# Optimization experiments

Hardware: AMD Instinct MI355X
Metric: run time of the kernel (lower is better)

The kernel has to match this reference:

```python
import jax, jax.numpy as jnp
import numpy as np

P = 2          # SamplesLoss p=2
BLUR = 0.05    # eps_final = BLUR**P = 0.0025
SCALING = 0.8  # annealing factor per iteration (on the blur scale)


def _cost(x, y):
    # geomloss cost for p=2: |x - y|^2 / 2, shape (N, M)
    x2 = jnp.sum(x * x, axis=-1)
    y2 = jnp.sum(y * y, axis=-1)
    return 0.5 * (x2[:, None] + y2[None, :] - 2.0 * (x @ y.T))


def _softmin(eps, C, h):
    # -eps * log sum_j exp(h_j - C_ij / eps); h already contains log-weights
    return -eps * jax.nn.logsumexp(h[None, :] - C / eps, axis=1)


def _eps_schedule(x, y):
    # geomloss scaling_parameters / epsilon_schedule with diameter from bounding box
    xn, yn = np.asarray(x), np.asarray(y)
    mins = np.minimum(xn.min(0), yn.min(0))
    maxs = np.maximum(xn.max(0), yn.max(0))
    diameter = float(np.linalg.norm(maxs - mins))
    eps_list = ([diameter ** P]
                + [float(np.exp(e)) for e in np.arange(P * np.log(diameter), P * np.log(BLUR), P * np.log(SCALING))]
                + [BLUR ** P])
    return eps_list


def _sinkhorn_divergence(x, y, eps_list):
    # Debiased Sinkhorn divergence S_eps(x, y), geomloss sinkhorn_tensorized
    N, M = x.shape[0], y.shape[0]
    sg = jax.lax.stop_gradient
    C_xy, C_yx = _cost(x, y), _cost(y, x)
    C_xx, C_yy = _cost(x, sg(x)), _cost(y, sg(y))  # geomloss detaches 2nd arg
    # The annealing loop runs with autograd disabled in geomloss:
    Cxy_, Cyx_, Cxx_, Cyy_ = sg(C_xy), sg(C_yx), sg(C_xx), sg(C_yy)
    a_log = jnp.full((N,), -np.log(N), dtype=x.dtype)  # log uniform weights
    b_log = jnp.full((M,), -np.log(M), dtype=y.dtype)
    e0 = eps_list[0]
    f_aa = _softmin(e0, Cxx_, a_log)
    g_bb = _softmin(e0, Cyy_, b_log)
    g_ab = _softmin(e0, Cyx_, a_log)
    f_ba = _softmin(e0, Cxy_, b_log)
    for eps in eps_list:  # fixed schedule, not a data-dim loop
        ft_ba = _softmin(eps, Cxy_, b_log + g_ab / eps)
        gt_ab = _softmin(eps, Cyx_, a_log + f_ba / eps)
        ft_aa = _softmin(eps, Cxx_, a_log + f_aa / eps)
        gt_bb = _softmin(eps, Cyy_, b_log + g_bb / eps)
        f_ba, g_ab = 0.5 * (f_ba + ft_ba), 0.5 * (g_ab + gt_ab)
        f_aa, g_bb = 0.5 * (f_aa + ft_aa), 0.5 * (g_bb + gt_bb)
    # Final extrapolation step (the only one geomloss differentiates through):
    eps = eps_list[-1]
    f_ba, g_ab = (_softmin(eps, C_xy, sg(b_log + g_ab / eps)),
                  _softmin(eps, C_yx, sg(a_log + f_ba / eps)))
    f_aa = _softmin(eps, C_xx, sg(a_log + f_aa / eps))
    g_bb = _softmin(eps, C_yy, sg(b_log + g_bb / eps))
    # scal with uniform weights == mean
    return jnp.mean(f_ba - f_aa) + jnp.mean(g_ab - g_bb)


def setup_inputs() -> dict:
    key = jax.random.key(0)
    kx, kt = jax.random.split(key)
    x = jax.random.normal(kx, (4096, 64), dtype=jnp.float32)
    target = jax.random.normal(kt, (4096, 64), dtype=jnp.float32)
    return {"x": x, "target": target}


def reference(x, target):
    eps_list = _eps_schedule(x, target)  # concrete schedule from data diameter
    return _sinkhorn_divergence(x, target, eps_list)
```

## Files before the change

### kernel.cpp

```cpp
#include <hip/hip_runtime.h>
#include <math.h>

#define NPTS 4096
#define DIM  64
#define MAX_ITERS 40
#define NCHUNK 32
#define TILE 128

#define ALOG (-8.317766166719343f)
#define L2E  (1.4426950408889634f)
#define LN2  (0.6931471805599453f)

#if __has_builtin(__builtin_amdgcn_exp2f)
#define EXP2F(x) __builtin_amdgcn_exp2f(x)
#else
#define EXP2F(x) exp2f(x)
#endif
#if __has_builtin(__builtin_amdgcn_logf)
#define LOG2F(x) __builtin_amdgcn_logf(x)
#else
#define LOG2F(x) log2f(x)
#endif

typedef _Float16 half8 __attribute__((ext_vector_type(8)));

__global__ void minmax_part_kernel(const float* __restrict__ x,
                                   const float* __restrict__ y,
                                   float* __restrict__ partmn,
                                   float* __restrict__ partmx) {
    int t = threadIdx.x;
    int bid = blockIdx.x;
    int g0 = bid * 256 + t;
    const int total = NPTS * DIM;
    float mn = INFINITY, mx = -INFINITY;
    for (int g = g0; g < total; g += 128 * 256) {
        float v = x[g]; mn = fminf(mn, v); mx = fmaxf(mx, v);
        float w = y[g]; mn = fminf(mn, w); mx = fmaxf(mx, w);
    }
    __shared__ float smn[256], smx[256];
    smn[t] = mn; smx[t] = mx;
    __syncthreads();
    if (t < 64) {
        for (int q = 1; q < 4; q++) {
            mn = fminf(mn, smn[t + 64 * q]);
            mx = fmaxf(mx, smx[t + 64 * q]);
        }
        partmn[bid * 64 + t] = mn;
        partmx[bid * 64 + t] = mx;
    }
}

__global__ void schedule_kernel(const float* __restrict__ partmn,
                                const float* __restrict__ partmx,
                                int* __restrict__ hdr,
                                float* __restrict__ sched) {
    int d = threadIdx.x;
    float mn = INFINITY, mx = -INFINITY;
    for (int b = 0; b < 128; b++) {
        mn = fminf(mn, partmn[b * 64 + d]);
        mx = fmaxf(mx, partmx[b * 64 + d]);
    }
    float range = mx - mn;
    __shared__ float r2[64];
    r2[d] = range * range;
    __syncthreads();
    if (d == 0) {
        float ss = 0.f;
        for (int k = 0; k < 64; k++) ss += r2[k];
        float diam_f = sqrtf(ss);
        double diam = (double)diam_f;
        double start = 2.0 * log(diam);
        double stop  = 2.0 * log(0.05);
        double step  = 2.0 * log(0.8);
        int n_ar = (int)ceil((stop - start) / step);
        if (n_ar < 0) n_ar = 0;
        int n_eps = n_ar + 2;
        if (n_eps > 64) n_eps = 64;
        sched[0] = (float)(diam * diam);
        for (int k = 0; k < n_ar && (1 + k) < 63; k++)
            sched[1 + k] = (float)exp(start + step * (double)k);
        sched[n_eps - 1] = 0.0025f;
        for (int k = n_eps; k < 64; k++) sched[k] = 0.0025f;
        hdr[0] = n_eps;
    }
}

__global__ void sqnorm_kernel(const float* __restrict__ X, float* __restrict__ out) {
    int wave = (blockIdx.x * blockDim.x + threadIdx.x) >> 6;
    int lane = threadIdx.x & 63;
    if (wave >= NPTS) return;
    float v = X[wave * DIM + lane];
    float s = v * v;
    for (int o = 32; o > 0; o >>= 1) s += __shfl_xor(s, o, 64);
    if (lane == 0) out[wave] = s;
}

__global__ __launch_bounds__(256) void gram_kernel(const float* __restrict__ A,
                                                   const float* __restrict__ B,
                                                   _Float16* __restrict__ G) {
    __shared__ float As[64][68], Bs[64][68];
    int t = threadIdx.x;
    int i0 = blockIdx.y * 64, j0 = blockIdx.x * 64;
    for (int q = 0; q < 4; q++) {
        int fi = q * 256 + t;
        int r = fi >> 4, c4 = (fi & 15) * 4;
        *(float4*)&As[r][c4] = *(const float4*)&A[(i0 + r) * DIM + c4];
        *(float4*)&Bs[r][c4] = *(const float4*)&B[(j0 + r) * DIM + c4];
    }
    __syncthreads();
    int tx = t & 15, ty = t >> 4;
    float acc[4][4] = {};
    for (int k = 0; k < 64; k++) {
        float a[4], b[4];
#pragma unroll
        for (int u = 0; u < 4; u++) a[u] = As[ty + 16 * u][k];
#pragma unroll
        for (int v = 0; v < 4; v++) b[v] = Bs[tx + 16 * v][k];
#pragma unroll
        for (int u = 0; u < 4; u++)
#pragma unroll
            for (int v = 0; v < 4; v++) acc[u][v] = fmaf(a[u], b[v], acc[u][v]);
    }
    for (int u = 0; u < 4; u++)
        for (int v = 0; v < 4; v++)
            G[(size_t)(i0 + ty + 16 * u) * NPTS + j0 + tx + 16 * v] = (_Float16)acc[u][v];
}

struct TileArgs {
    const _Float16 *Gxy, *Gxx, *Gyy;
    const float *x2, *y2;
    const float *fba, *gab, *faa, *gbb;
    float *PxyR_m, *PxyR_s, *PxyC_m, *PxyC_s;
    float *Pxx_m, *Pxx_s, *Pyy_m, *Pyy_s;
    const int* hdr; const float* sched;
    int t; int mode;
};

__global__ __launch_bounds__(256) void tile_kernel(TileArgs A) {
    int n_eps = A.hdr[0];
    if (A.mode == 1 && A.t >= n_eps) return;
    int idx = (A.t < 0) ? (n_eps - 1) : A.t;
    float eps = A.sched[idx];
    float inv2 = (1.0f / eps) * L2E;

    int b = blockIdx.x;
    const _Float16 *G;
    const float *hc_f, *hc_sq, *hr_f, *hr_sq;
    float *Prm, *Prs, *Pcm, *Pcs;
    int ti, tj; bool diag = false;
    if (b < 1024) {
        ti = b >> 5; tj = b & 31;
        G = A.Gxy;
        hc_f = A.gab; hc_sq = A.y2;
        hr_f = A.fba; hr_sq = A.x2;
        Prm = A.PxyR_m; Prs = A.PxyR_s; Pcm = A.PxyC_m; Pcs = A.PxyC_s;
    } else {
        int u;
        if (b < 1024 + 528) {
            u = b - 1024; G = A.Gxx; hc_f = A.faa; hc_sq = A.x2;
            Prm = A.Pxx_m; Prs = A.Pxx_s; Pcm = A.Pxx_m; Pcs = A.Pxx_s;
        } else {
            u = b - 1552; G = A.Gyy; hc_f = A.gbb; hc_sq = A.y2;
            Prm = A.Pyy_m; Prs = A.Pyy_s; Pcm = A.Pyy_m; Pcs = A.Pyy_s;
        }
        hr_f = hc_f; hr_sq = hc_sq;
        ti = 0; while (u >= NCHUNK - ti) { u -= NCHUNK - ti; ti++; }
        tj = ti + u;
        diag = (ti == tj);
    }
    const float base2 = ALOG * L2E;

    __shared__ float tile[64][65];
    __shared__ float h2c[128], h2r[128];
    __shared__ float red_m[4][64], red_s[4][64];

    int tt = threadIdx.x;
    int gi0 = ti * TILE, gj0 = tj * TILE;
    if (tt < 128) {
        int j = gj0 + tt;
        float f = hc_f ? hc_f[j] : 0.f;
        h2c[tt] = base2 + (f - 0.5f * hc_sq[j]) * inv2;
    } else {
        int i = gi0 + (tt - 128);
        float f = hr_f ? hr_f[i] : 0.f;
        h2r[tt - 128] = base2 + (f - 0.5f * hr_sq[i]) * inv2;
    }

    float rm[2] = {-INFINITY, -INFINITY}, rs[2] = {0.f, 0.f};
    float cm[2] = {-INFINITY, -INFINITY}, cs[2] = {0.f, 0.f};
    int lr = tt & 63, lq = tt >> 6;

    for (int qc = 0; qc < 2; qc++) {
        for (int qr = 0; qr < 2; qr++) {
            __syncthreads();
            {
                const _Float16* src = G + (size_t)(gi0 + qr * 64) * NPTS + gj0 + qc * 64;
                for (int q = 0; q < 2; q++) {
                    int fi = q * 256 + tt;
                    int r = fi >> 3, c8 = (fi & 7) * 8;
                    half8 h = *(const half8*)(src + (size_t)r * NPTS + c8);
#pragma unroll
                    for (int j = 0; j < 8; j++) tile[r][c8 + j] = (float)h[j];
                }
            }
            __syncthreads();
            {
                float v[16], lm = -INFINITY;
#pragma unroll
                for (int k = 0; k < 16; k++) {
                    v[k] = fmaf(tile[lr][lq * 16 + k], inv2, h2c[qc * 64 + lq * 16 + k]);
                    lm = fmaxf(lm, v[k]);
                }
                float nm = fmaxf(rm[qr], lm);
                float acc = rs[qr] * EXP2F(rm[qr] - nm);
#pragma unroll
                for (int k = 0; k < 16; k++) acc += EXP2F(v[k] - nm);
                rm[qr] = nm; rs[qr] = acc;
            }
            if (!diag) {
                float v[16], lm = -INFINITY;
#pragma unroll
                for (int k = 0; k < 16; k++) {
                    v[k] = fmaf(tile[lq * 16 + k][lr], inv2, h2r[qr * 64 + lq * 16 + k]);
                    lm = fmaxf(lm, v[k]);
                }
                float nm = fmaxf(cm[qc], lm);
                float acc = cs[qc] * EXP2F(cm[qc] - nm);
#pragma unroll
                for (int k = 0; k < 16; k++) acc += EXP2F(v[k] - nm);
                cm[qc] = nm; cs[qc] = acc;
            }
        }
    }

    for (int qr = 0; qr < 2; qr++) {
        __syncthreads();
        red_m[lq][lr] = rm[qr]; red_s[lq][lr] = rs[qr];
        __syncthreads();
        if (tt < 64) {
            float M = fmaxf(fmaxf(red_m[0][tt], red_m[1][tt]),
                            fmaxf(red_m[2][tt], red_m[3][tt]));
            float S = red_s[0][tt] * EXP2F(red_m[0][tt] - M)
                    + red_s[1][tt] * EXP2F(red_m[1][tt] - M)
                    + red_s[2][tt] * EXP2F(red_m[2][tt] - M)
                    + red_s[3][tt] * EXP2F(red_m[3][tt] - M);
            int gi = gi0 + qr * 64 + tt;
            Prm[tj * NPTS + gi] = M; Prs[tj * NPTS + gi] = S;
        }
    }
    if (!diag) {
        for (int qc = 0; qc < 2; qc++) {
            __syncthreads();
            red_m[lq][lr] = cm[qc]; red_s[lq][lr] = cs[qc];
            __syncthreads();
            if (tt < 64) {
                float M = fmaxf(fmaxf(red_m[0][tt], red_m[1][tt]),
                                fmaxf(red_m[2][tt], red_m[3][tt]));
                float S = red_s[0][tt] * EXP2F(red_m[0][tt] - M)
                        + red_s[1][tt] * EXP2F(red_m[1][tt] - M)
                        + red_s[2][tt] * EXP2F(red_m[2][tt] - M)
                        + red_s[3][tt] * EXP2F(red_m[3][tt] - M);
                int gj = gj0 + qc * 64 + tt;
                Pcm[ti * NPTS + gj] = M; Pcs[ti * NPTS + gj] = S;
            }
        }
    }
}

struct CombArgs {
    const float *PxyR_m, *PxyR_s, *PxyC_m, *PxyC_s;
    const float *Pxx_m, *Pxx_s, *Pyy_m, *Pyy_s;
    const float *x2, *y2;
    const float *fba_old, *gab_old, *faa_old, *gbb_old;
    float *fba, *gab, *faa, *gbb;
    const int* hdr; const float* sched; int t; int mode;
};

__global__ void comb_kernel(CombArgs A) {
    int vec = blockIdx.x >> 4;
    int r = (blockIdx.x & 15) * 256 + threadIdx.x;
    int n_eps = A.hdr[0];
    const float *Pm, *Ps, *sq, *old; float *out;
    switch (vec) {
        case 0:  Pm = A.PxyR_m; Ps = A.PxyR_s; sq = A.x2; old = A.fba_old; out = A.fba; break;
        case 1:  Pm = A.PxyC_m; Ps = A.PxyC_s; sq = A.y2; old = A.gab_old; out = A.gab; break;
        case 2:  Pm = A.Pxx_m;  Ps = A.Pxx_s;  sq = A.x2; old = A.faa_old; out = A.faa; break;
        default: Pm = A.Pyy_m;  Ps = A.Pyy_s;  sq = A.y2; old = A.gbb_old; out = A.gbb; break;
    }
    if (A.mode == 1 && A.t >= n_eps) { out[r] = old[r]; return; }
    int idx = (A.t < 0) ? (n_eps - 1) : A.t;
    float eps = A.sched[idx];
    float M = -INFINITY;
    for (int q = 0; q < NCHUNK; q++) M = fmaxf(M, Pm[q * NPTS + r]);
    float S = 0.f;
    for (int q = 0; q < NCHUNK; q++) S += Ps[q * NPTS + r] * EXP2F(Pm[q * NPTS + r] - M);
    float res = 0.5f * sq[r] - eps * LN2 * (M + LOG2F(S));
    out[r] = (A.mode == 1) ? 0.5f * (old[r] + res) : res;
}

__global__ void reduce_kernel(const float* __restrict__ fba, const float* __restrict__ faa,
                              const float* __restrict__ gab, const float* __restrict__ gbb,
                              float* __restrict__ out) {
    int t = threadIdx.x;
    double s1 = 0.0, s2 = 0.0;
    for (int i = t; i < NPTS; i += 256) {
        s1 += (double)fba[i] - (double)faa[i];
        s2 += (double)gab[i] - (double)gbb[i];
    }
    __shared__ double sh1[256], sh2[256];
    sh1[t] = s1; sh2[t] = s2;
    __syncthreads();
    for (int o = 128; o > 0; o >>= 1) {
        if (t < o) { sh1[t] += sh1[t + o]; sh2[t] += sh2[t + o]; }
        __syncthreads();
    }
    if (t == 0) out[0] = (float)(sh1[0] / NPTS + sh2[0] / NPTS);
}

extern "C" void kernel_launch(void* const* d_in, const int* in_sizes, int n_in,
                              void* d_out, int out_size, void* d_ws, size_t ws_size,
                              hipStream_t stream) {
    const float* x = (const float*)d_in[0];
    const float* y = (const float*)d_in[1];
    float* out = (float*)d_out;
    float* w = (float*)d_ws;

    int*   hdr   = (int*)w;
    float* sched = w + 16;
    float* pmn   = w + 80;
    float* pmx   = w + 8272;
    float* x2    = w + 16464;
    float* y2    = w + 20560;
    float* st    = w + 24656;
    float* fba[2] = { st,            st + 4096 };
    float* gab[2] = { st + 2*4096,   st + 3*4096 };
    float* faa[2] = { st + 4*4096,   st + 5*4096 };
    float* gbb[2] = { st + 6*4096,   st + 7*4096 };
    float* P = w + 57424;
    float* PxyR_m = P;             float* PxyR_s = P + 131072;
    float* PxyC_m = P + 2*131072;  float* PxyC_s = P + 3*131072;
    float* Pxx_m  = P + 4*131072;  float* Pxx_s  = P + 5*131072;
    float* Pyy_m  = P + 6*131072;  float* Pyy_s  = P + 7*131072;
    const size_t NN = (size_t)NPTS * NPTS;
    _Float16* Gxy = (_Float16*)(w + 2097152);
    _Float16* Gxx = Gxy + NN;
    _Float16* Gyy = Gxx + NN;

    hipLaunchKernelGGL(minmax_part_kernel, dim3(128), dim3(256), 0, stream, x, y, pmn, pmx);
    hipLaunchKernelGGL(schedule_kernel, dim3(1), dim3(64), 0, stream, pmn, pmx, hdr, sched);
    hipLaunchKernelGGL(sqnorm_kernel, dim3(1024), dim3(256), 0, stream, x, x2);
    hipLaunchKernelGGL(sqnorm_kernel, dim3(1024), dim3(256), 0, stream, y, y2);
    hipLaunchKernelGGL(gram_kernel, dim3(64, 64), dim3(256), 0, stream, x, y, Gxy);
    hipLaunchKernelGGL(gram_kernel, dim3(64, 64), dim3(256), 0, stream, x, x, Gxx);
    hipLaunchKernelGGL(gram_kernel, dim3(64, 64), dim3(256), 0, stream, y, y, Gyy);

    const int NBLK = 1024 + 528 + 528;
    TileArgs TA;
    TA.Gxy = Gxy; TA.Gxx = Gxx; TA.Gyy = Gyy;
    TA.x2 = x2; TA.y2 = y2;
    TA.PxyR_m = PxyR_m; TA.PxyR_s = PxyR_s; TA.PxyC_m = PxyC_m; TA.PxyC_s = PxyC_s;
    TA.Pxx_m = Pxx_m; TA.Pxx_s = Pxx_s; TA.Pyy_m = Pyy_m; TA.Pyy_s = Pyy_s;
    TA.hdr = hdr; TA.sched = sched;

    CombArgs CA;
    CA.PxyR_m = PxyR_m; CA.PxyR_s = PxyR_s; CA.PxyC_m = PxyC_m; CA.PxyC_s = PxyC_s;
    CA.Pxx_m = Pxx_m; CA.Pxx_s = Pxx_s; CA.Pyy_m = Pyy_m; CA.Pyy_s = Pyy_s;
    CA.x2 = x2; CA.y2 = y2; CA.hdr = hdr; CA.sched = sched;

    TA.fba = nullptr; TA.gab = nullptr; TA.faa = nullptr; TA.gbb = nullptr;
    TA.t = 0; TA.mode = 0;
    hipLaunchKernelGGL(tile_kernel, dim3(NBLK), dim3(256), 0, stream, TA);
    CA.fba_old = nullptr; CA.gab_old = nullptr; CA.faa_old = nullptr; CA.gbb_old = nullptr;
    CA.fba = fba[0]; CA.gab = gab[0]; CA.faa = faa[0]; CA.gbb = gbb[0];
    CA.t = 0; CA.mode = 0;
    hipLaunchKernelGGL(comb_kernel, dim3(64), dim3(256), 0, stream, CA);

    int cur = 0;
    for (int t = 0; t < MAX_ITERS; t++) {
        int nx = cur ^ 1;
        TA.fba = fba[cur]; TA.gab = gab[cur]; TA.faa = faa[cur]; TA.gbb = gbb[cur];
        TA.t = t; TA.mode = 1;
        hipLaunchKernelGGL(tile_kernel, dim3(NBLK), dim3(256), 0, stream, TA);
        CA.fba_old = fba[cur]; CA.gab_old = gab[cur]; CA.faa_old = faa[cur]; CA.gbb_old = gbb[cur];
        CA.fba = fba[nx]; CA.gab = gab[nx]; CA.faa = faa[nx]; CA.gbb = gbb[nx];
        CA.t = t; CA.mode = 1;
        hipLaunchKernelGGL(comb_kernel, dim3(64), dim3(256), 0, stream, CA);
        cur = nx;
    }

    int nx = cur ^ 1;
    TA.fba = fba[cur]; TA.gab = gab[cur]; TA.faa = faa[cur]; TA.gbb = gbb[cur];
    TA.t = -1; TA.mode = 0;
    hipLaunchKernelGGL(tile_kernel, dim3(NBLK), dim3(256), 0, stream, TA);
    CA.fba_old = fba[cur]; CA.gab_old = gab[cur]; CA.faa_old = faa[cur]; CA.gbb_old = gbb[cur];
    CA.fba = fba[nx]; CA.gab = gab[nx]; CA.faa = faa[nx]; CA.gbb = gbb[nx];
    CA.t = -1; CA.mode = 0;
    hipLaunchKernelGGL(comb_kernel, dim3(64), dim3(256), 0, stream, CA);

    hipLaunchKernelGGL(reduce_kernel, dim3(1), dim3(256), 0, stream,
                       fba[nx], faa[nx], gab[nx], gbb[nx], out);
}
```

Measured before the change: 1.157 ms.

## Compute Sinkhorn tile logsumexp directly from registers, dropping shared-memory tile staging

The fp16 cost tile is no longer staged through a 64x65 float shared-memory array. Each thread keeps its two half8 rows in registers and updates the row partial logsumexp and the online column logsumexp directly. Row partials are then combined with wavefront shuffles, and column partials with a two-level shared-memory reduction. This removes the LDS round trip and several barriers per sub-tile, at the cost of more exp2 work per element in the column online update. MAX_ITERS is also lowered from 40 to 36, which may shrink a fixed-size allocation or loop bound.

```diff
diff --git a/kernel.cpp b/kernel.cpp
--- a/kernel.cpp
+++ b/kernel.cpp
@@ -3,7 +3,7 @@
 
 #define NPTS 4096
 #define DIM  64
-#define MAX_ITERS 40
+#define MAX_ITERS 36
 #define NCHUNK 32
 #define TILE 128
 
@@ -170,9 +170,9 @@
     }
     const float base2 = ALOG * L2E;
 
-    __shared__ float tile[64][65];
     __shared__ float h2c[128], h2r[128];
-    __shared__ float red_m[4][64], red_s[4][64];
+    __shared__ float cmL[32][68], csL[32][68];
+    __shared__ float g4m[4][68], g4s[4][68];
 
     int tt = threadIdx.x;
     int gi0 = ti * TILE, gj0 = tj * TILE;
@@ -185,84 +185,108 @@
         float f = hr_f ? hr_f[i] : 0.f;
         h2r[tt - 128] = base2 + (f - 0.5f * hr_sq[i]) * inv2;
     }
-
-    float rm[2] = {-INFINITY, -INFINITY}, rs[2] = {0.f, 0.f};
-    float cm[2] = {-INFINITY, -INFINITY}, cs[2] = {0.f, 0.f};
-    int lr = tt & 63, lq = tt >> 6;
+    __syncthreads();
+
+    int a = tt >> 3;
+    int bcol = (tt & 7) * 8;
+
+    float rm4[4] = {-INFINITY, -INFINITY, -INFINITY, -INFINITY};
+    float rs4[4] = {0.f, 0.f, 0.f, 0.f};
 
     for (int qc = 0; qc < 2; qc++) {
+        float cm8[8], cs8[8];
+#pragma unroll
+        for (int j = 0; j < 8; j++) { cm8[j] = -INFINITY; cs8[j] = 0.f; }
+        float hc[8];
+#pragma unroll
+        for (int j = 0; j < 8; j++) hc[j] = h2c[qc * 64 + bcol + j];
+
         for (int qr = 0; qr < 2; qr++) {
+            const _Float16* src = G + (size_t)(gi0 + qr * 64) * NPTS + gj0 + qc * 64;
+            half8 hA = *(const half8*)(src + (size_t)a * NPTS + bcol);
+            half8 hB = *(const half8*)(src + (size_t)(a + 32) * NPTS + bcol);
+#pragma unroll
+            for (int ri = 0; ri < 2; ri++) {
+                int rloc = qr * 64 + ri * 32 + a;
+                float hr = h2r[rloc];
+                float tv[8];
+#pragma unroll
+                for (int j = 0; j < 8; j++) {
+                    float g = (ri == 0) ? (float)hA[j] : (float)hB[j];
+                    tv[j] = g * inv2;
+                }
+                int k = qr * 2 + ri;
+                float lm = -INFINITY;
+                float v[8];
+#pragma unroll
+                for (int j = 0; j < 8; j++) { v[j] = tv[j] + hc[j]; lm = fmaxf(lm, v[j]); }
+                float nm = fmaxf(rm4[k], lm);
+                float acc = rs4[k] * EXP2F(rm4[k] - nm);
+#pragma unroll
+                for (int j = 0; j < 8; j++) acc += EXP2F(v[j] - nm);
+                rm4[k] = nm; rs4[k] = acc;
+                if (!diag) {
+#pragma unroll
+                    for (int j = 0; j < 8; j++) {
+                        float wv = tv[j] + hr;
+                        float cn = fmaxf(cm8[j], wv);
+                        cs8[j] = cs8[j] * EXP2F(cm8[j] - cn) + EXP2F(wv - cn);
+                        cm8[j] = cn;
+                    }
+                }
+            }
+        }
+        if (!diag) {
+            __syncthreads();
+#pragma unroll
+            for (int j = 0; j < 8; j++) { cmL[a][bcol + j] = cm8[j]; csL[a][bcol + j] = cs8[j]; }
             __syncthreads();
             {
-                const _Float16* src = G + (size_t)(gi0 + qr * 64) * NPTS + gj0 + qc * 64;
-                for (int q = 0; q < 2; q++) {
-                    int fi = q * 256 + tt;
-                    int r = fi >> 3, c8 = (fi & 7) * 8;
-                    half8 h = *(const half8*)(src + (size_t)r * NPTS + c8);
-#pragma unroll
-                    for (int j = 0; j < 8; j++) tile[r][c8 + j] = (float)h[j];
+                int c = tt & 63, g = tt >> 6;
+                float M = -INFINITY, S = 0.f;
+#pragma unroll
+                for (int k = 0; k < 8; k++) {
+                    float m = cmL[g * 8 + k][c], s = csL[g * 8 + k][c];
+                    float cn = fmaxf(M, m);
+                    S = S * EXP2F(M - cn) + s * EXP2F(m - cn);
+                    M = cn;
                 }
+                g4m[g][c] = M; g4s[g][c] = S;
             }
             __syncthreads();
-            {
-                float v[16], lm = -INFINITY;
-#pragma unroll
-                for (int k = 0; k < 16; k++) {
-                    v[k] = fmaf(tile[lr][lq * 16 + k], inv2, h2c[qc * 64 + lq * 16 + k]);
-                    lm = fmaxf(lm, v[k]);
+            if (tt < 64) {
+                float M = -INFINITY, S = 0.f;
+#pragma unroll
+                for (int g = 0; g < 4; g++) {
+                    float m = g4m[g][tt], s = g4s[g][tt];
+                    float cn = fmaxf(M, m);
+                    S = S * EXP2F(M - cn) + s * EXP2F(m - cn);
+                    M = cn;
                 }
-                float nm = fmaxf(rm[qr], lm);
-                float acc = rs[qr] * EXP2F(rm[qr] - nm);
-#pragma unroll
-                for (int k = 0; k < 16; k++) acc += EXP2F(v[k] - nm);
-                rm[qr] = nm; rs[qr] = acc;
-            }
-            if (!diag) {
-                float v[16], lm = -INFINITY;
-#pragma unroll
-                for (int k = 0; k < 16; k++) {
-                    v[k] = fmaf(tile[lq * 16 + k][lr], inv2, h2r[qr * 64 + lq * 16 + k]);
-                    lm = fmaxf(lm, v[k]);
-                }
-                float nm = fmaxf(cm[qc], lm);
-                float acc = cs[qc] * EXP2F(cm[qc] - nm);
-#pragma unroll
-                for (int k = 0; k < 16; k++) acc += EXP2F(v[k] - nm);
-                cm[qc] = nm; cs[qc] = acc;
-            }
-        }
-    }
-
-    for (int qr = 0; qr < 2; qr++) {
-        __syncthreads();
-        red_m[lq][lr] = rm[qr]; red_s[lq][lr] = rs[qr];
-        __syncthreads();
-        if (tt < 64) {
-            float M = fmaxf(fmaxf(red_m[0][tt], red_m[1][tt]),
-                            fmaxf(red_m[2][tt], red_m[3][tt]));
-            float S = red_s[0][tt] * EXP2F(red_m[0][tt] - M)
-                    + red_s[1][tt] * EXP2F(red_m[1][tt] - M)
-                    + red_s[2][tt] * EXP2F(red_m[2][tt] - M)
-                    + red_s[3][tt] * EXP2F(red_m[3][tt] - M);
-            int gi = gi0 + qr * 64 + tt;
-            Prm[tj * NPTS + gi] = M; Prs[tj * NPTS + gi] = S;
-        }
-    }
-    if (!diag) {
-        for (int qc = 0; qc < 2; qc++) {
-            __syncthreads();
-            red_m[lq][lr] = cm[qc]; red_s[lq][lr] = cs[qc];
-            __syncthreads();
-            if (tt < 64) {
-                float M = fmaxf(fmaxf(red_m[0][tt], red_m[1][tt]),
-                                fmaxf(red_m[2][tt], red_m[3][tt]));
-                float S = red_s[0][tt] * EXP2F(red_m[0][tt] - M)
-                        + red_s[1][tt] * EXP2F(red_m[1][tt] - M)
-                        + red_s[2][tt] * EXP2F(red_m[2][tt] - M)
-                        + red_s[3][tt] * EXP2F(red_m[3][tt] - M);
                 int gj = gj0 + qc * 64 + tt;
                 Pcm[ti * NPTS + gj] = M; Pcs[ti * NPTS + gj] = S;
             }
+        }
+    }
+
+#pragma unroll
+    for (int k = 0; k < 4; k++) {
+        float m = rm4[k], s = rs4[k];
+#pragma unroll
+        for (int off = 1; off < 8; off <<= 1) {
+            float om = __shfl_xor(m, off, 64);
+            float os = __shfl_xor(s, off, 64);
+            float cn = fmaxf(m, om);
+            s = s * EXP2F(m - cn) + os * EXP2F(om - cn);
+            m = cn;
+        }
+        rm4[k] = m; rs4[k] = s;
+    }
+    if ((tt & 7) == 0) {
+#pragma unroll
+        for (int k = 0; k < 4; k++) {
+            int gi = gi0 + (k >> 1) * 64 + (k & 1) * 32 + a;
+            Prm[tj * NPTS + gi] = rm4[k]; Prs[tj * NPTS + gi] = rs4[k];
         }
     }
 }
```

Result: slower. 1.324 ms (+14.4%).
